# Kernel optimization log

Measured on AMD Instinct MI355X. Metric: run time of the kernel, lower is better.

The kernel has to match this reference:

```python
import jax, jax.numpy as jnp
import numpy as np

N_NODES = 100000
N_EDGES = 1600000
N_GRAPHS = 512
HID = 200
IN_DIM = 205
EPS = 1e-5


def _bn(x, g, b, m, v):
    # inference-mode BatchNorm1d
    return (x - m) * (g / jnp.sqrt(v + EPS)) + b


def setup_inputs() -> dict:
    key = jax.random.key(0)
    ks = jax.random.split(key, 12)
    d = {}
    d['x'] = jax.random.normal(ks[0], (N_NODES, IN_DIM), dtype=jnp.float32)
    d['edge_index'] = jax.random.randint(ks[1], (2, N_EDGES), 0, N_NODES, dtype=jnp.int64)
    d['batch'] = jnp.sort(jax.random.randint(ks[2], (N_NODES,), 0, N_GRAPHS, dtype=jnp.int64))
    s = 0.05
    d['proj_W'] = jax.random.normal(ks[3], (HID, IN_DIM), dtype=jnp.float32) * s
    d['proj_b'] = jax.random.normal(ks[4], (HID,), dtype=jnp.float32) * s
    for p, i in (('bn1', 0), ('bn2', 1), ('bnf', 2)):
        d[p + '_g'] = jnp.ones((HID,), jnp.float32)
        d[p + '_b'] = jnp.zeros((HID,), jnp.float32)
        d[p + '_m'] = jnp.zeros((HID,), jnp.float32)
        d[p + '_v'] = jnp.ones((HID,), jnp.float32)
    d['ggc_W'] = jax.random.normal(ks[5], (3, HID, HID), dtype=jnp.float32) * s
    d['gru_wih'] = jax.random.normal(ks[6], (3 * HID, HID), dtype=jnp.float32) * s
    d['gru_whh'] = jax.random.normal(ks[7], (3 * HID, HID), dtype=jnp.float32) * s
    d['gru_bih'] = jax.random.normal(ks[8], (3 * HID,), dtype=jnp.float32) * s
    d['gru_bhh'] = jax.random.normal(ks[9], (3 * HID,), dtype=jnp.float32) * s
    d['fc1_W'] = jax.random.normal(ks[10], (HID, 2 * HID), dtype=jnp.float32) * s
    d['fc1_b'] = jnp.zeros((HID,), jnp.float32)
    d['fc2_W'] = jax.random.normal(ks[11], (2, HID), dtype=jnp.float32) * s
    d['fc2_b'] = jnp.zeros((2,), jnp.float32)
    return d


def _gru_cell(m, h, wih, whh, bih, bhh):
    gi = m @ wih.T + bih   # [N, 3H] gates from input, order r,z,n
    gh = h @ whh.T + bhh
    ir, iz, inn = jnp.split(gi, 3, axis=-1)
    hr, hz, hn = jnp.split(gh, 3, axis=-1)
    r = jax.nn.sigmoid(ir + hr)
    z = jax.nn.sigmoid(iz + hz)
    n = jnp.tanh(inn + r * hn)
    return (1.0 - z) * n + z * h


def reference(x, edge_index, batch, proj_W, proj_b,
              bn1_g, bn1_b, bn1_m, bn1_v,
              ggc_W, gru_wih, gru_whh, gru_bih, gru_bhh,
              bn2_g, bn2_b, bn2_m, bn2_v,
              fc1_W, fc1_b, bnf_g, bnf_b, bnf_m, bnf_v,
              fc2_W, fc2_b):
    src, dst = edge_index[0], edge_index[1]
    h = x @ proj_W.T + proj_b                      # [N, H]
    h = jax.nn.relu(_bn(h, bn1_g, bn1_b, bn1_m, bn1_v))
    # GatedGraphConv: 3 steps of (linear -> scatter-add over edges -> GRU)
    for i in range(3):
        m = h @ ggc_W[i]                           # [N, H]
        agg = jax.ops.segment_sum(m[src], dst, num_segments=N_NODES)
        h = _gru_cell(agg, h, gru_wih, gru_whh, gru_bih, gru_bhh)
    h = jax.nn.relu(_bn(h, bn2_g, bn2_b, bn2_m, bn2_v))
    # dual pooling per graph
    cnt = jax.ops.segment_sum(jnp.ones((h.shape[0],), h.dtype), batch, num_segments=N_GRAPHS)
    x_mean = jax.ops.segment_sum(h, batch, num_segments=N_GRAPHS) / jnp.maximum(cnt, 1.0)[:, None]
    x_max = jax.ops.segment_max(h, batch, num_segments=N_GRAPHS)
    x_max = jnp.where(cnt[:, None] > 0, x_max, 0.0)
    g = jnp.concatenate([x_mean, x_max], axis=1)   # [G, 2H]
    g = g @ fc1_W.T + fc1_b
    g = jax.nn.relu(_bn(g, bnf_g, bnf_b, bnf_m, bnf_v))
    return g @ fc2_W.T + fc2_b                     # [G, 2]
```

## Files before the change

### kernel.cpp

```cpp
#include <hip/hip_runtime.h>
#include <cmath>

#define NN 100000
#define NE 1600000
#define NG 512
#define H 200
#define D 205
#define EPSV 1e-5f
#define SCAN_B 1024
#define KP 224
#define LPH 208

typedef __attribute__((ext_vector_type(8))) short short8v;
typedef __attribute__((ext_vector_type(4))) float f32x4;

#define MFMA16(a,b,c) __builtin_amdgcn_mfma_f32_16x16x32_bf16(a,b,c,0,0,0)

static __device__ __forceinline__ float sigm(float x){ return 1.0f/(1.0f+expf(-x)); }

static __device__ __forceinline__ void split2(float x, unsigned short& h, unsigned short& l){
  unsigned xb = __float_as_uint(x);
  h = (unsigned short)(xb >> 16);
  float hf = __uint_as_float(xb & 0xffff0000u);
  l = (unsigned short)(__float_as_uint(x - hf) >> 16);
}

static __device__ __forceinline__ float uf(unsigned short u){
  return __uint_as_float(((unsigned)u) << 16);
}

static __device__ __forceinline__ void gload16(const void* src, void* dst){
  __builtin_amdgcn_global_load_lds(
      (const __attribute__((address_space(1))) unsigned int*)src,
      (__attribute__((address_space(3))) unsigned int*)dst, 16, 0, 0);
}

__global__ __launch_bounds__(256) void cvt_split(const float* __restrict__ in,
    unsigned short* __restrict__ hi, unsigned short* __restrict__ lo, int rows, int C, int P){
  long i = (long)blockIdx.x*256 + threadIdx.x;
  long tot = (long)rows*P;
  if (i >= tot) return;
  int r = (int)(i/P), c = (int)(i - (long)r*P);
  float v = (c < C) ? in[(size_t)r*C + c] : 0.f;
  unsigned short hh, ll; split2(v,hh,ll);
  hi[i] = hh; lo[i] = ll;
}

__global__ __launch_bounds__(256) void cvt_tsplit(const float* __restrict__ in,
    unsigned short* __restrict__ hi, unsigned short* __restrict__ lo, int R, int C){
  int i = blockIdx.x*256 + threadIdx.x;
  if (i >= C*KP) return;
  int n = i/KP, k = i - n*KP;
  float v = (k < R) ? in[(size_t)k*C + n] : 0.f;
  unsigned short hh, ll; split2(v,hh,ll);
  hi[i] = hh; lo[i] = ll;
}

template<int EPIL>
__global__ __launch_bounds__(256) void mgemm(
    const unsigned short* __restrict__ Ahi, const unsigned short* __restrict__ Alo,
    const unsigned short* __restrict__ Bhi, const unsigned short* __restrict__ Blo,
    int M, int N, int nj, int npan,
    const float* __restrict__ bias,
    const float* __restrict__ bg, const float* __restrict__ bb,
    const float* __restrict__ bm, const float* __restrict__ bv,
    unsigned short* __restrict__ Chi, unsigned short* __restrict__ Clo,
    float* __restrict__ Cf)
{
  __shared__ __align__(16) char S[16384];
  const int bid = blockIdx.x;
  const int xcd = bid & 7, sl = bid >> 3;
  const int pl = sl / nj, jj = sl - pl*nj;
  const int p = pl*8 + xcd;
  if (p >= npan) return;
  const int n0 = jj*128, r0 = p*128;
  const int tid = threadIdx.x, lane = tid & 63, wave = tid >> 6;
  const int wr = (wave>>1)*64, wc = (wave&1)*64;
  const int fr = lane & 15, fq = lane >> 4;
  f32x4 acc[4][4] = {};

  const unsigned short* sp[4]; int sdst[4];
  #pragma unroll
  for (int i = 0; i < 4; ++i) {
    int g = wave + 4*i;
    int region = g >> 3, c = g & 7, rowgrp = c >> 2, q = c & 3;
    int row = rowgrp*64 + lane;
    int rg = n0 + row; if (rg > N-1) rg = N-1;
    sp[i] = (region ? Blo : Bhi) + (size_t)rg*KP + q*8;
    sdst[i] = region*8192 + q*2048 + rowgrp*1024;
  }
  int arow[4];
  #pragma unroll
  for (int t = 0; t < 4; ++t) {
    int rg = r0 + wr + t*16 + fr; if (rg > M-1) rg = M-1;
    arow[t] = rg*LPH + fq*8;
  }

  for (int k0 = 0; k0 < KP; k0 += 32) {
    #pragma unroll
    for (int i = 0; i < 4; ++i) gload16(sp[i] + k0, S + sdst[i]);
    __syncthreads();
    short8v ah[4], al[4], bh[4], bl[4];
    #pragma unroll
    for (int t = 0; t < 4; ++t) {
      ah[t] = *(const short8v*)(Ahi + arow[t] + k0);
      al[t] = *(const short8v*)(Alo + arow[t] + k0);
      int rb = (wc + t*16 + fr)*16;
      bh[t] = *(const short8v*)(S +    0 + fq*2048 + rb);
      bl[t] = *(const short8v*)(S + 8192 + fq*2048 + rb);
    }
    #pragma unroll
    for (int i = 0; i < 4; ++i)
      #pragma unroll
      for (int j = 0; j < 4; ++j) {
        acc[i][j] = MFMA16(ah[i], bh[j], acc[i][j]);
        acc[i][j] = MFMA16(ah[i], bl[j], acc[i][j]);
        acc[i][j] = MFMA16(al[i], bh[j], acc[i][j]);
      }
    __syncthreads();
  }

  #pragma unroll
  for (int i = 0; i < 4; ++i)
    #pragma unroll
    for (int j = 0; j < 4; ++j)
      #pragma unroll
      for (int q = 0; q < 4; ++q) {
        int row = r0 + wr + i*16 + fq*4 + q;
        int col = n0 + wc + j*16 + fr;
        if (row < M && col < N) {
          float c = acc[i][j][q];
          if (EPIL) {
            c += bias[col];
            c = (c - bm[col]) * (bg[col] * rsqrtf(bv[col] + EPSV)) + bb[col];
            c = fmaxf(c, 0.f);
            unsigned short hh, ll; split2(c, hh, ll);
            size_t o = (size_t)row*LPH + col;
            Chi[o] = hh; Clo[o] = ll;
          } else {
            Cf[(size_t)row*LPH + col] = c;
          }
        } else if (EPIL && row < M && col >= N && col < LPH) {
          size_t o = (size_t)row*LPH + col;
          Chi[o] = 0; Clo[o] = 0;
        }
      }
}

__global__ __launch_bounds__(256, 3) void gru6(
    const unsigned short* __restrict__ Ghi, const unsigned short* __restrict__ Glo,
    const unsigned short* __restrict__ Hhi, const unsigned short* __restrict__ Hlo,
    const unsigned short* __restrict__ Wihh, const unsigned short* __restrict__ Wihl,
    const unsigned short* __restrict__ Whhh, const unsigned short* __restrict__ Whhl,
    const float* __restrict__ bih, const float* __restrict__ bhh,
    int nj, int npan,
    unsigned short* __restrict__ Ohi, unsigned short* __restrict__ Olo)
{
  __shared__ __align__(16) char S[24576];
  const int bid = blockIdx.x;
  const int xcd = bid & 7, sl = bid >> 3;
  const int pl = sl / nj, jt = sl - pl*nj;
  const int p = pl*8 + xcd;
  if (p >= npan) return;
  const int j0 = jt*32, r0 = p*128;
  const int tid = threadIdx.x, lane = tid & 63, wave = tid >> 6;
  const int fr = lane & 15, fq = lane >> 4;
  f32x4 acc[4][2][2] = {};

  const unsigned short* sp[6]; int sdst[6];
  #pragma unroll
  for (int i = 0; i < 6; ++i) {
    int g = wave + 4*i;
    int comp = g / 12, c = g - comp*12, rowgrp = c >> 2, q = c & 3;
    int R = rowgrp*64 + lane, gate = R>>5, jjj = R&31;
    int g3 = (gate >= 3) ? gate-3 : gate;
    int jcol = j0 + jjj; if (jcol > H-1) jcol = H-1;
    const unsigned short* base = (gate < 3) ? (comp ? Wihl : Wihh) : (comp ? Whhl : Whhh);
    sp[i] = base + (size_t)(g3*H + jcol)*KP + q*8;
    sdst[i] = comp*12288 + q*3072 + rowgrp*1024;
  }
  int arow[2];
  #pragma unroll
  for (int t = 0; t < 2; ++t) {
    int rg = r0 + wave*32 + t*16 + fr; if (rg > NN-1) rg = NN-1;
    arow[t] = rg*LPH + fq*8;
  }

  for (int k0 = 0; k0 < KP; k0 += 32) {
    #pragma unroll
    for (int i = 0; i < 6; ++i) gload16(sp[i] + k0, S + sdst[i]);
    __syncthreads();
    short8v A[4][2];
    #pragma unroll
    for (int t = 0; t < 2; ++t) {
      A[0][t] = *(const short8v*)(Ghi + arow[t] + k0);
      A[1][t] = *(const short8v*)(Glo + arow[t] + k0);
      A[2][t] = *(const short8v*)(Hhi + arow[t] + k0);
      A[3][t] = *(const short8v*)(Hlo + arow[t] + k0);
    }
    #pragma unroll
    for (int g = 0; g < 6; ++g) {
      const char* w0 = S +     0 + fq*3072;
      const char* w1 = S + 12288 + fq*3072;
      short8v b0h = *(const short8v*)(w0 + (g*32      + fr)*16);
      short8v b1h = *(const short8v*)(w0 + (g*32 + 16 + fr)*16);
      short8v b0l = *(const short8v*)(w1 + (g*32      + fr)*16);
      short8v b1l = *(const short8v*)(w1 + (g*32 + 16 + fr)*16);
      const int ai = (g < 3) ? 0 : 2;
      const int ac = (g == 5) ? 3 : (g % 3);
      #pragma unroll
      for (int t = 0; t < 2; ++t) {
        acc[ac][t][0] = MFMA16(A[ai][t],   b0h, acc[ac][t][0]);
        acc[ac][t][0] = MFMA16(A[ai][t],   b0l, acc[ac][t][0]);
        acc[ac][t][0] = MFMA16(A[ai+1][t], b0h, acc[ac][t][0]);
        acc[ac][t][1] = MFMA16(A[ai][t],   b1h, acc[ac][t][1]);
        acc[ac][t][1] = MFMA16(A[ai][t],   b1l, acc[ac][t][1]);
        acc[ac][t][1] = MFMA16(A[ai+1][t], b1h, acc[ac][t][1]);
      }
    }
    __syncthreads();
  }

  #pragma unroll
  for (int ct = 0; ct < 2; ++ct) {
    int j = j0 + ct*16 + fr;
    if (j >= LPH) continue;
    if (j >= H) {
      #pragma unroll
      for (int t = 0; t < 2; ++t)
        #pragma unroll
        for (int q = 0; q < 4; ++q) {
          int row = r0 + wave*32 + t*16 + fq*4 + q;
          if (row >= NN) continue;
          size_t o = (size_t)row*LPH + j;
          Ohi[o] = 0; Olo[o] = 0;
        }
      continue;
    }
    float br  = bih[j]     + bhh[j];
    float bz  = bih[H+j]   + bhh[H+j];
    float bin = bih[2*H+j], bhn = bhh[2*H+j];
    #pragma unroll
    for (int t = 0; t < 2; ++t)
      #pragma unroll
      for (int q = 0; q < 4; ++q) {
        int row = r0 + wave*32 + t*16 + fq*4 + q;
        if (row >= NN) continue;
        float rv = sigm(acc[0][t][ct][q] + br);
        float zv = sigm(acc[1][t][ct][q] + bz);
        float nv = tanhf(acc[2][t][ct][q] + bin + rv*(acc[3][t][ct][q] + bhn));
        size_t o = (size_t)row*LPH + j;
        float ho = uf(Hhi[o]) + uf(Hlo[o]);
        unsigned short hh2, ll2; split2((1.f - zv)*nv + zv*ho, hh2, ll2);
        Ohi[o] = hh2; Olo[o] = ll2;
      }
  }
}

__global__ __launch_bounds__(256) void hist_k(const int* __restrict__ dst, int* __restrict__ deg){
  int e = blockIdx.x*256 + threadIdx.x;
  if (e < NE) atomicAdd(&deg[dst[e]], 1);
}

__global__ __launch_bounds__(256) void scan1_k(const int* __restrict__ deg, int* __restrict__ part,
                                               int* __restrict__ bsum, int n){
  __shared__ int lds[256];
  int t = threadIdx.x;
  int base = blockIdx.x * SCAN_B + t*4;
  int v[4]; int s = 0;
  #pragma unroll
  for (int q = 0; q < 4; ++q){ int idx = base+q; v[q] = (idx < n) ? deg[idx] : 0; s += v[q]; }
  lds[t] = s;
  __syncthreads();
  for (int off = 1; off < 256; off <<= 1){
    int val = 0;
    if (t >= off) val = lds[t-off];
    __syncthreads();
    if (t >= off) lds[t] += val;
    __syncthreads();
  }
  if (t == 255) bsum[blockIdx.x] = lds[255];
  int run = (t == 0) ? 0 : lds[t-1];
  #pragma unroll
  for (int q = 0; q < 4; ++q){ int idx = base+q; if (idx < n) part[idx] = run; run += v[q]; }
}

__global__ void scan2_k(int* __restrict__ bsum, int nb){
  __shared__ int lds[128];
  int t = threadIdx.x;
  int v = (t < nb) ? bsum[t] : 0;
  lds[t] = v;
  __syncthreads();
  for (int off = 1; off < 128; off <<= 1){
    int val = 0;
    if (t >= off) val = lds[t-off];
    __syncthreads();
    if (t >= off) lds[t] += val;
    __syncthreads();
  }
  if (t < nb) bsum[t] = (t == 0) ? 0 : lds[t-1];
}

__global__ __launch_bounds__(256) void scan3_k(const int* __restrict__ part, const int* __restrict__ bsum,
                                               int* __restrict__ rowptr, int* __restrict__ cpos, int n){
  int i = blockIdx.x*256 + threadIdx.x;
  if (i < n){
    int v = part[i] + bsum[i >> 10];
    rowptr[i] = v;
    cpos[i] = v;
  }
  if (i == 0) rowptr[n] = NE;
}

__global__ __launch_bounds__(256) void fill_k(const int* __restrict__ src, const int* __restrict__ dst,
                                              int* __restrict__ cpos, int* __restrict__ elist){
  int e = blockIdx.x*256 + threadIdx.x;
  if (e < NE){
    int p = atomicAdd(&cpos[dst[e]], 1);
    elist[p] = src[e];
  }
}

__global__ __launch_bounds__(256) void gather_k(const float* __restrict__ m,
                                                const int* __restrict__ rowptr,
                                                const int* __restrict__ elist,
                                                unsigned short* __restrict__ ahi,
                                                unsigned short* __restrict__ alo){
  __shared__ int sIdx[256];
  int n = blockIdx.x;
  int beg = rowptr[n], end = rowptr[n+1];
  int j = threadIdx.x;
  float a0=0.f, a1=0.f, a2=0.f, a3=0.f;
  for (int c0 = beg; c0 < end; c0 += 256){
    int cnt = min(256, end - c0);
    __syncthreads();
    if (threadIdx.x < cnt) sIdx[threadIdx.x] = elist[c0 + threadIdx.x];
    __syncthreads();
    if (j < H){
      int k = 0;
      for (; k + 4 <= cnt; k += 4){
        a0 += m[(size_t)sIdx[k  ]*LPH + j];
        a1 += m[(size_t)sIdx[k+1]*LPH + j];
        a2 += m[(size_t)sIdx[k+2]*LPH + j];
        a3 += m[(size_t)sIdx[k+3]*LPH + j];
      }
      for (; k < cnt; ++k){
        a0 += m[(size_t)sIdx[k]*LPH + j];
      }
    }
  }
  if (j < H){
    unsigned short hh, ll; split2((a0 + a1) + (a2 + a3), hh, ll);
    size_t o = (size_t)n*LPH + j;
    ahi[o] = hh; alo[o] = ll;
  }
}

__global__ __launch_bounds__(256) void pool_g(
    const unsigned short* __restrict__ hhi, const unsigned short* __restrict__ hlo,
    const int* __restrict__ batch,
    const float* __restrict__ g2, const float* __restrict__ b2,
    const float* __restrict__ m2, const float* __restrict__ v2,
    float* __restrict__ gmean, float* __restrict__ gmax)
{
  int g = blockIdx.x;
  int lo = 0, hi = NN;
  while (lo < hi){ int mid = (lo+hi)>>1; if (batch[mid] < g) lo = mid+1; else hi = mid; }
  int lo2 = lo, hi2 = NN;
  while (lo2 < hi2){ int mid = (lo2+hi2)>>1; if (batch[mid] < g+1) lo2 = mid+1; else hi2 = mid; }
  int j = threadIdx.x;
  if (j >= H) return;
  float s = g2[j] * rsqrtf(v2[j] + EPSV);
  float mm = m2[j], bb = b2[j];
  float sum = 0.f, mx = 0.f;
  for (int n = lo; n < hi2; ++n){
    size_t o = (size_t)n*LPH + j;
    float hv = uf(hhi[o]) + uf(hlo[o]);
    float val = fmaxf((hv - mm)*s + bb, 0.f);
    sum += val;
    mx = fmaxf(mx, val);
  }
  int c = hi2 - lo;
  gmean[g*H + j] = (c > 0) ? sum/(float)c : 0.f;
  gmax [g*H + j] = mx;
}

__global__ __launch_bounds__(256) void fc1_k(
    const float* __restrict__ gmean, const float* __restrict__ gmax,
    const float* __restrict__ W,
    const float* __restrict__ bias,
    const float* __restrict__ fg, const float* __restrict__ fb,
    const float* __restrict__ fm, const float* __restrict__ fv,
    float* __restrict__ out)
{
  int tid = blockIdx.x*256 + threadIdx.x;
  if (tid >= NG*H) return;
  int g = tid / H, j = tid - g*H;
  const float* wr = W + j*2*H;
  float acc = bias[j];
  for (int k = 0; k < H; ++k) acc += gmean[g*H + k] * wr[k];
  for (int k = 0; k < H; ++k) acc += gmax[g*H + k] * wr[H + k];
  float s = fg[j] * rsqrtf(fv[j] + EPSV);
  acc = (acc - fm[j]) * s + fb[j];
  out[tid] = fmaxf(acc, 0.f);
}

__global__ void fc2_k(const float* __restrict__ in, const float* __restrict__ W,
                      const float* __restrict__ bias, float* __restrict__ out)
{
  int tid = blockIdx.x*256 + threadIdx.x;
  if (tid >= NG*2) return;
  int g = tid >> 1, c = tid & 1;
  float acc = bias[c];
  const float* wr = W + c*H;
  const float* xr = in + g*H;
  for (int k = 0; k < H; ++k) acc += xr[k]*wr[k];
  out[tid] = acc;
}

extern "C" void kernel_launch(void* const* d_in, const int* in_sizes, int n_in,
                              void* d_out, int out_size, void* d_ws, size_t ws_size,
                              hipStream_t stream)
{
  const float* x     = (const float*)d_in[0];
  const int*   eidx  = (const int*)d_in[1];
  const int*   batch = (const int*)d_in[2];
  const float* projW = (const float*)d_in[3];
  const float* projb = (const float*)d_in[4];
  const float* bn1g  = (const float*)d_in[5];
  const float* bn1b  = (const float*)d_in[6];
  const float* bn1m  = (const float*)d_in[7];
  const float* bn1v  = (const float*)d_in[8];
  const float* bn2g  = (const float*)d_in[9];
  const float* bn2b  = (const float*)d_in[10];
  const float* bn2m  = (const float*)d_in[11];
  const float* bn2v  = (const float*)d_in[12];
  const float* bnfg  = (const float*)d_in[13];
  const float* bnfb  = (const float*)d_in[14];
  const float* bnfm  = (const float*)d_in[15];
  const float* bnfv  = (const float*)d_in[16];
  const float* ggcW  = (const float*)d_in[17];
  const float* wih   = (const float*)d_in[18];
  const float* whh   = (const float*)d_in[19];
  const float* bih   = (const float*)d_in[20];
  const float* bhh   = (const float*)d_in[21];
  const float* fc1W  = (const float*)d_in[22];
  const float* fc1b  = (const float*)d_in[23];
  const float* fc2W  = (const float*)d_in[24];
  const float* fc2b  = (const float*)d_in[25];

  char* wsp = (char*)d_ws;
  auto alloc = [&](size_t nbytes) {
    char* p = wsp;
    wsp += ((nbytes + 255) / 256) * 256;
    return (void*)p;
  };
  const size_t PAIRE = (size_t)NN*LPH;
  unsigned short* xaHi = (unsigned short*)alloc(PAIRE*4);
  unsigned short* xaLo = xaHi + PAIRE;
  char* grd0 = (char*)alloc(256);
  unsigned short* hHi  = (unsigned short*)alloc(PAIRE*4);
  unsigned short* hLo  = hHi + PAIRE;
  char* grd1 = (char*)alloc(256);
  unsigned short* mHi  = (unsigned short*)alloc(PAIRE*4);
  unsigned short* mLo  = mHi + PAIRE;
  char* grd2 = (char*)alloc(256);
  unsigned short* pBh   = (unsigned short*)alloc((size_t)H*KP*2);
  unsigned short* pBl   = (unsigned short*)alloc((size_t)H*KP*2);
  unsigned short* wihBh = (unsigned short*)alloc((size_t)3*H*KP*2);
  unsigned short* wihBl = (unsigned short*)alloc((size_t)3*H*KP*2);
  unsigned short* whhBh = (unsigned short*)alloc((size_t)3*H*KP*2);
  unsigned short* whhBl = (unsigned short*)alloc((size_t)3*H*KP*2);
  unsigned short* gBh[3]; unsigned short* gBl[3];
  for (int i = 0; i < 3; ++i) {
    gBh[i] = (unsigned short*)alloc((size_t)H*KP*2);
    gBl[i] = (unsigned short*)alloc((size_t)H*KP*2);
  }
  float* gmean = (float*)alloc((size_t)NG*H*4);
  float* gmax  = (float*)alloc((size_t)NG*H*4);
  float* fc1o  = (float*)alloc((size_t)NG*H*4);
  const int NB = (NN + SCAN_B - 1) / SCAN_B;
  int* deg    = (int*)alloc((size_t)NN*4);
  int* part   = (int*)alloc((size_t)NN*4);
  int* bsum   = (int*)alloc((size_t)NB*4);
  int* rowptr = (int*)alloc((size_t)(NN+1)*4);
  int* cpos   = (int*)alloc((size_t)NN*4);
  int* elist  = (int*)alloc((size_t)NE*4);

  const int* srcp = eidx;
  const int* dstp = eidx + NE;

  hipMemsetAsync(grd0, 0, 256, stream);
  hipMemsetAsync(grd1, 0, 256, stream);
  hipMemsetAsync(grd2, 0, 256, stream);

  hipMemsetAsync(deg, 0, (size_t)NN*4, stream);
  hist_k<<<(NE + 255)/256, 256, 0, stream>>>(dstp, deg);
  scan1_k<<<NB, 256, 0, stream>>>(deg, part, bsum, NN);
  scan2_k<<<1, 128, 0, stream>>>(bsum, NB);
  scan3_k<<<(NN + 255)/256, 256, 0, stream>>>(part, bsum, rowptr, cpos, NN);
  fill_k<<<(NE + 255)/256, 256, 0, stream>>>(srcp, dstp, cpos, elist);

  cvt_split<<<(int)(((long)H*KP + 255)/256), 256, 0, stream>>>(projW, pBh, pBl, H, D, KP);
  cvt_split<<<(int)(((long)3*H*KP + 255)/256), 256, 0, stream>>>(wih, wihBh, wihBl, 3*H, H, KP);
  cvt_split<<<(int)(((long)3*H*KP + 255)/256), 256, 0, stream>>>(whh, whhBh, whhBl, 3*H, H, KP);
  for (int i = 0; i < 3; ++i)
    cvt_tsplit<<<(H*KP + 255)/256, 256, 0, stream>>>(ggcW + (size_t)i*H*H, gBh[i], gBl[i], H, H);

  cvt_split<<<(int)(((long)NN*LPH + 255)/256), 256, 0, stream>>>(x, xaHi, xaLo, NN, D, LPH);

  const int NPAN = (NN + 127)/128;
  const int PL8  = (NPAN + 7)/8;
  const int NJ_G = (H + 127)/128;
  const int NJ_U = (H + 31)/32;
  const int GRID_G = 8 * NJ_G * PL8;
  const int GRID_U = 8 * NJ_U * PL8;

  mgemm<1><<<GRID_G, 256, 0, stream>>>(xaHi, xaLo, pBh, pBl, NN, H, NJ_G, NPAN,
                                       projb, bn1g, bn1b, bn1m, bn1v, hHi, hLo, nullptr);

  unsigned short *chHi = hHi, *chLo = hLo, *cmHi = mHi, *cmLo = mLo;
  for (int i = 0; i < 3; ++i) {
    float* mF = (float*)cmHi;
    mgemm<0><<<GRID_G, 256, 0, stream>>>(chHi, chLo, gBh[i], gBl[i], NN, H, NJ_G, NPAN,
                                         nullptr, nullptr, nullptr, nullptr, nullptr,
                                         nullptr, nullptr, mF);
    gather_k<<<NN, 256, 0, stream>>>(mF, rowptr, elist, xaHi, xaLo);
    gru6<<<GRID_U, 256, 0, stream>>>(xaHi, xaLo, chHi, chLo,
                                     wihBh, wihBl, whhBh, whhBl,
                                     bih, bhh, NJ_U, NPAN, cmHi, cmLo);
    unsigned short* t;
    t = chHi; chHi = cmHi; cmHi = t;
    t = chLo; chLo = cmLo; cmLo = t;
  }

  pool_g<<<NG, 256, 0, stream>>>(chHi, chLo, batch, bn2g, bn2b, bn2m, bn2v, gmean, gmax);
  fc1_k<<<(NG*H + 255)/256, 256, 0, stream>>>(gmean, gmax, fc1W, fc1b,
                                              bnfg, bnfb, bnfm, bnfv, fc1o);
  fc2_k<<<(NG*2 + 255)/256, 256, 0, stream>>>(fc1o, fc2W, fc2b, (float*)d_out);
}
```

Before: 2.122 ms.

## Double-buffer LDS and prefetch A fragments in mgemm and gru6 k-loops

Both GEMM kernels (mgemm and gru6) now use two LDS buffers and issue the next k-slice's global-to-LDS loads and A-fragment register loads before the current slice's MFMAs. This lets global load latency overlap with compute and removes one barrier per iteration's dependency stall. It doubles LDS use and adds prefetch registers, and gru6's launch bound drops from 3 to 2 blocks per CU to make room, which lowers occupancy.

```diff
diff --git a/kernel.cpp b/kernel.cpp
--- a/kernel.cpp
+++ b/kernel.cpp
@@ -67,7 +67,7 @@
     unsigned short* __restrict__ Chi, unsigned short* __restrict__ Clo,
     float* __restrict__ Cf)
 {
-  __shared__ __align__(16) char S[16384];
+  __shared__ __align__(16) char S[2][16384];
   const int bid = blockIdx.x;
   const int xcd = bid & 7, sl = bid >> 3;
   const int pl = sl / nj, jj = sl - pl*nj;
@@ -96,28 +96,48 @@
     arow[t] = rg*LPH + fq*8;
   }
 
-  for (int k0 = 0; k0 < KP; k0 += 32) {
-    #pragma unroll
-    for (int i = 0; i < 4; ++i) gload16(sp[i] + k0, S + sdst[i]);
-    __syncthreads();
-    short8v ah[4], al[4], bh[4], bl[4];
+  short8v AH[4], AL[4], NH[4], NL[4];
+  #pragma unroll
+  for (int i = 0; i < 4; ++i) gload16(sp[i], S[0] + sdst[i]);
+  #pragma unroll
+  for (int t = 0; t < 4; ++t) {
+    AH[t] = *(const short8v*)(Ahi + arow[t]);
+    AL[t] = *(const short8v*)(Alo + arow[t]);
+  }
+  __syncthreads();
+
+  for (int kk = 0; kk < 7; ++kk) {
+    const int kb = kk & 1;
+    if (kk < 6) {
+      const int kn = (kk+1)*32;
+      #pragma unroll
+      for (int i = 0; i < 4; ++i) gload16(sp[i] + kn, S[kb^1] + sdst[i]);
+      #pragma unroll
+      for (int t = 0; t < 4; ++t) {
+        NH[t] = *(const short8v*)(Ahi + arow[t] + kn);
+        NL[t] = *(const short8v*)(Alo + arow[t] + kn);
+      }
+    }
+    short8v bh[4], bl[4];
     #pragma unroll
     for (int t = 0; t < 4; ++t) {
-      ah[t] = *(const short8v*)(Ahi + arow[t] + k0);
-      al[t] = *(const short8v*)(Alo + arow[t] + k0);
       int rb = (wc + t*16 + fr)*16;
-      bh[t] = *(const short8v*)(S +    0 + fq*2048 + rb);
-      bl[t] = *(const short8v*)(S + 8192 + fq*2048 + rb);
+      bh[t] = *(const short8v*)(S[kb] +    0 + fq*2048 + rb);
+      bl[t] = *(const short8v*)(S[kb] + 8192 + fq*2048 + rb);
     }
     #pragma unroll
     for (int i = 0; i < 4; ++i)
       #pragma unroll
       for (int j = 0; j < 4; ++j) {
-        acc[i][j] = MFMA16(ah[i], bh[j], acc[i][j]);
-        acc[i][j] = MFMA16(ah[i], bl[j], acc[i][j]);
-        acc[i][j] = MFMA16(al[i], bh[j], acc[i][j]);
-      }
-    __syncthreads();
+        acc[i][j] = MFMA16(AH[i], bh[j], acc[i][j]);
+        acc[i][j] = MFMA16(AH[i], bl[j], acc[i][j]);
+        acc[i][j] = MFMA16(AL[i], bh[j], acc[i][j]);
+      }
+    __syncthreads();
+    if (kk < 6) {
+      #pragma unroll
+      for (int t = 0; t < 4; ++t) { AH[t] = NH[t]; AL[t] = NL[t]; }
+    }
   }
 
   #pragma unroll
@@ -147,7 +167,7 @@
       }
 }
 
-__global__ __launch_bounds__(256, 3) void gru6(
+__global__ __launch_bounds__(256, 2) void gru6(
     const unsigned short* __restrict__ Ghi, const unsigned short* __restrict__ Glo,
     const unsigned short* __restrict__ Hhi, const unsigned short* __restrict__ Hlo,
     const unsigned short* __restrict__ Wihh, const unsigned short* __restrict__ Wihl,
@@ -156,7 +176,7 @@
     int nj, int npan,
     unsigned short* __restrict__ Ohi, unsigned short* __restrict__ Olo)
 {
-  __shared__ __align__(16) char S[24576];
+  __shared__ __align__(16) char S[2][24576];
   const int bid = blockIdx.x;
   const int xcd = bid & 7, sl = bid >> 3;
   const int pl = sl / nj, jt = sl - pl*nj;
@@ -186,22 +206,36 @@
     arow[t] = rg*LPH + fq*8;
   }
 
-  for (int k0 = 0; k0 < KP; k0 += 32) {
-    #pragma unroll
-    for (int i = 0; i < 6; ++i) gload16(sp[i] + k0, S + sdst[i]);
-    __syncthreads();
-    short8v A[4][2];
-    #pragma unroll
-    for (int t = 0; t < 2; ++t) {
-      A[0][t] = *(const short8v*)(Ghi + arow[t] + k0);
-      A[1][t] = *(const short8v*)(Glo + arow[t] + k0);
-      A[2][t] = *(const short8v*)(Hhi + arow[t] + k0);
-      A[3][t] = *(const short8v*)(Hlo + arow[t] + k0);
-    }
+  short8v Ac[4][2], An[4][2];
+  #pragma unroll
+  for (int i = 0; i < 6; ++i) gload16(sp[i], S[0] + sdst[i]);
+  #pragma unroll
+  for (int t = 0; t < 2; ++t) {
+    Ac[0][t] = *(const short8v*)(Ghi + arow[t]);
+    Ac[1][t] = *(const short8v*)(Glo + arow[t]);
+    Ac[2][t] = *(const short8v*)(Hhi + arow[t]);
+    Ac[3][t] = *(const short8v*)(Hlo + arow[t]);
+  }
+  __syncthreads();
+
+  for (int kk = 0; kk < 7; ++kk) {
+    const int kb = kk & 1;
+    if (kk < 6) {
+      const int kn = (kk+1)*32;
+      #pragma unroll
+      for (int i = 0; i < 6; ++i) gload16(sp[i] + kn, S[kb^1] + sdst[i]);
+      #pragma unroll
+      for (int t = 0; t < 2; ++t) {
+        An[0][t] = *(const short8v*)(Ghi + arow[t] + kn);
+        An[1][t] = *(const short8v*)(Glo + arow[t] + kn);
+        An[2][t] = *(const short8v*)(Hhi + arow[t] + kn);
+        An[3][t] = *(const short8v*)(Hlo + arow[t] + kn);
+      }
+    }
+    const char* w0 = S[kb] +     0 + fq*3072;
+    const char* w1 = S[kb] + 12288 + fq*3072;
     #pragma unroll
     for (int g = 0; g < 6; ++g) {
-      const char* w0 = S +     0 + fq*3072;
-      const char* w1 = S + 12288 + fq*3072;
       short8v b0h = *(const short8v*)(w0 + (g*32      + fr)*16);
       short8v b1h = *(const short8v*)(w0 + (g*32 + 16 + fr)*16);
       short8v b0l = *(const short8v*)(w1 + (g*32      + fr)*16);
@@ -210,15 +244,21 @@
       const int ac = (g == 5) ? 3 : (g % 3);
       #pragma unroll
       for (int t = 0; t < 2; ++t) {
-        acc[ac][t][0] = MFMA16(A[ai][t],   b0h, acc[ac][t][0]);
-        acc[ac][t][0] = MFMA16(A[ai][t],   b0l, acc[ac][t][0]);
-        acc[ac][t][0] = MFMA16(A[ai+1][t], b0h, acc[ac][t][0]);
-        acc[ac][t][1] = MFMA16(A[ai][t],   b1h, acc[ac][t][1]);
-        acc[ac][t][1] = MFMA16(A[ai][t],   b1l, acc[ac][t][1]);
-        acc[ac][t][1] = MFMA16(A[ai+1][t], b1h, acc[ac][t][1]);
-      }
-    }
-    __syncthreads();
+        acc[ac][t][0] = MFMA16(Ac[ai][t],   b0h, acc[ac][t][0]);
+        acc[ac][t][0] = MFMA16(Ac[ai][t],   b0l, acc[ac][t][0]);
+        acc[ac][t][0] = MFMA16(Ac[ai+1][t], b0h, acc[ac][t][0]);
+        acc[ac][t][1] = MFMA16(Ac[ai][t],   b1h, acc[ac][t][1]);
+        acc[ac][t][1] = MFMA16(Ac[ai][t],   b1l, acc[ac][t][1]);
+        acc[ac][t][1] = MFMA16(Ac[ai+1][t], b1h, acc[ac][t][1]);
+      }
+    }
+    __syncthreads();
+    if (kk < 6) {
+      #pragma unroll
+      for (int c2 = 0; c2 < 4; ++c2)
+        #pragma unroll
+        for (int t = 0; t < 2; ++t) Ac[c2][t] = An[c2][t];
+    }
   }
 
   #pragma unroll
```

After: 1.961 ms. -7.6%, faster.
